# Kernel tuning notes

Hardware: AMD Instinct MI355X
Metric: run time of the kernel (lower is better)

## Reference

```python
import jax, jax.numpy as jnp
import numpy as np

N_NODES = 100000
N_EDGES = 1600000
D = 32  # atom and bond feature dim


def _mlp(x, W1, b1, W2, b2, W3, b3):
    # fff: Linear(in,128) -> ReLU -> Linear(128,64) -> ReLU -> Linear(64,32)
    h = jax.nn.relu(x @ W1 + b1)
    h = jax.nn.relu(h @ W2 + b2)
    return h @ W3 + b3


def _init_mlp(key, in_dim):
    ks = jax.random.split(key, 3)
    def lin(k, fan_in, fan_out):
        bound = 1.0 / np.sqrt(fan_in)
        kw, kb = jax.random.split(k)
        W = jax.random.uniform(kw, (fan_in, fan_out), jnp.float32, -bound, bound)
        b = jax.random.uniform(kb, (fan_out,), jnp.float32, -bound, bound)
        return W, b
    W1, b1 = lin(ks[0], in_dim, 128)
    W2, b2 = lin(ks[1], 128, 64)
    W3, b3 = lin(ks[2], 64, 32)
    return W1, b1, W2, b2, W3, b3


def setup_inputs() -> dict:
    key = jax.random.key(0)
    k_bonds, k_a1, k_a2, k_atoms, k_e, k_v = jax.random.split(key, 6)
    inp = {
        "bonds": jax.random.normal(k_bonds, (N_EDGES, D), jnp.float32),
        "bond_atom_1": jax.random.randint(k_a1, (N_EDGES,), 0, N_NODES, jnp.int64),
        "bond_atom_2": jax.random.randint(k_a2, (N_EDGES,), 0, N_NODES, jnp.int64),
        "atoms": jax.random.normal(k_atoms, (N_NODES, D), jnp.float32),
    }
    We1, be1, We2, be2, We3, be3 = _init_mlp(k_e, 96)
    Wv1, bv1, Wv2, bv2, Wv3, bv3 = _init_mlp(k_v, 64)
    inp.update(We1=We1, be1=be1, We2=We2, be2=be2, We3=We3, be3=be3,
               Wv1=Wv1, bv1=bv1, Wv2=Wv2, bv2=bv2, Wv3=Wv3, bv3=bv3)
    return inp


def reference(bonds, bond_atom_1, bond_atom_2, atoms,
              We1, be1, We2, be2, We3, be3,
              Wv1, bv1, Wv2, bv2, Wv3, bv3):
    # Edge update: gather endpoint atom features, concat with bond feats, MLP
    atom1 = atoms[bond_atom_1]                    # [E, D]
    atom2 = atoms[bond_atom_2]                    # [E, D]
    e_in = jnp.concatenate([atom1, atom2, bonds], axis=1)  # [E, 3D]
    new_bonds = _mlp(e_in, We1, be1, We2, be2, We3, be3)    # [E, 32]

    # Node update: scatter-mean new bond features onto target atoms
    # (PyG default flow aggregates messages at edge_index[1] == bond_atom_2)
    n = atoms.shape[0]
    seg_sum = jax.ops.segment_sum(new_bonds, bond_atom_2, num_segments=n)
    counts = jax.ops.segment_sum(jnp.ones((new_bonds.shape[0],), new_bonds.dtype),
                                 bond_atom_2, num_segments=n)
    mean_bonds = seg_sum / jnp.maximum(counts, 1.0)[:, None]  # [N, 32]

    v_in = jnp.concatenate([mean_bonds, atoms], axis=1)        # [N, 64]
    new_atoms = _mlp(v_in, Wv1, bv1, Wv2, bv2, Wv3, bv3)       # [N, 32]
    return (new_atoms, new_bonds)
```

## Files before the change

kernel.cpp:

```cpp
#include <hip/hip_runtime.h>
#include <hip/hip_bf16.h>

#define NN 100000
#define NE 1600000
#define NB_SCAN 391
#define ETILES 12500
#define EGRID 768
#define NGRID 1024

typedef __attribute__((ext_vector_type(8))) short bfrag8;
typedef __attribute__((ext_vector_type(4))) float f32x4;
typedef __attribute__((ext_vector_type(8))) unsigned short us8;
typedef __attribute__((ext_vector_type(4))) unsigned int u32x4;

__device__ __forceinline__ unsigned short f2bf(float f) {
  unsigned int u = __float_as_uint(f);
  u += 0x7fffu + ((u >> 16) & 1u);
  return (unsigned short)(u >> 16);
}

__device__ __forceinline__ unsigned int pk2(float a, float b) {
  unsigned int r;
  asm("v_cvt_pk_bf16_f32 %0, %1, %2" : "=v"(r) : "v"(a), "v"(b));
  return r;
}

__device__ __forceinline__ uint2 pk4(float v0, float v1, float v2, float v3) {
  return make_uint2(pk2(v0, v1), pk2(v2, v3));
}

__device__ __forceinline__ bfrag8 pack8(float4 a, float4 b) {
  union { u32x4 u; bfrag8 f; } c;
  c.u[0] = pk2(a.x, a.y); c.u[1] = pk2(a.z, a.w);
  c.u[2] = pk2(b.x, b.y); c.u[3] = pk2(b.z, b.w);
  return c.f;
}

__device__ __forceinline__ bfrag8 as_frag(us8 v) {
  union { us8 u; bfrag8 f; } c;
  c.u = v;
  return c.f;
}

__device__ __forceinline__ bfrag8 as_frag_u(u32x4 v) {
  union { u32x4 u; bfrag8 f; } c;
  c.u = v;
  return c.f;
}

__device__ __forceinline__ unsigned int sh(unsigned int v, int src) {
  return (unsigned int)__shfl((int)v, src, 64);
}

__device__ __forceinline__ float bl(unsigned int u) { return __uint_as_float(u << 16); }
__device__ __forceinline__ float bh(unsigned int u) { return __uint_as_float(u & 0xffff0000u); }

__device__ __forceinline__ f32x4 mfma16(bfrag8 a, bfrag8 b, f32x4 c) {
  return __builtin_amdgcn_mfma_f32_16x16x32_bf16(a, b, c, 0, 0, 0);
}

__device__ __forceinline__ void gload_lds16(const void* g, void* l) {
  __builtin_amdgcn_global_load_lds(
      (const __attribute__((address_space(1))) unsigned int*)g,
      (__attribute__((address_space(3))) unsigned int*)l, 16, 0, 0);
}

__global__ void prep(const float* __restrict__ atoms, unsigned short* __restrict__ atoms_bf,
                     const int* __restrict__ a2, int* __restrict__ cnt,
                     const float* __restrict__ We1, const float* __restrict__ We2,
                     const float* __restrict__ We3, const float* __restrict__ Wv1,
                     const float* __restrict__ Wv2, const float* __restrict__ Wv3,
                     unsigned short* __restrict__ wp) {
  const int b = blockIdx.x, tid = threadIdx.x;
  if (b < 3125) {
    const int i = b * 256 + tid;
    float4 v = *(const float4*)(atoms + (size_t)i * 4);
    *(uint2*)(atoms_bf + (size_t)i * 4) = pk4(v.x, v.y, v.z, v.w);
  } else if (b < 3125 + 6250) {
    const int e = (b - 3125) * 256 + tid;
    if (e < NE) atomicAdd(&cnt[a2[e]], 1);
  } else {
    const int i = (b - 9375) * 256 + tid;
    const float* src; int base, N;
    if (i < 12288)      { src = We1; base = 0;     N = 128; }
    else if (i < 20480) { src = We2; base = 12288; N = 64;  }
    else if (i < 22528) { src = We3; base = 20480; N = 32;  }
    else if (i < 30720) { src = Wv1; base = 22528; N = 128; }
    else if (i < 38912) { src = Wv2; base = 30720; N = 64;  }
    else                { src = Wv3; base = 38912; N = 32;  }
    const int il = i - base;
    const int j = il & 7, gc = il >> 3;
    const int c = gc % N, g = gc / N;
    wp[i] = f2bf(src[(g * 8 + j) * N + c]);
  }
}

__global__ void scan_blocks(const int* __restrict__ cnt, int* __restrict__ off,
                            int* __restrict__ bsum) {
  __shared__ int s[256];
  const int t = threadIdx.x;
  const int idx = blockIdx.x * 256 + t;
  int v = (idx < NN) ? cnt[idx] : 0;
  s[t] = v;
  __syncthreads();
  for (int d = 1; d < 256; d <<= 1) {
    int x = (t >= d) ? s[t - d] : 0;
    __syncthreads();
    s[t] += x;
    __syncthreads();
  }
  if (idx < NN) off[idx] = s[t] - v;
  if (t == 255) bsum[blockIdx.x] = s[255];
}

__global__ void scan_finalize(int* __restrict__ off, const int* __restrict__ bsum,
                              int* __restrict__ cursor) {
  __shared__ int red[256];
  const int b = blockIdx.x, t = threadIdx.x;
  int s = 0;
  for (int k = t; k < b; k += 256) s += bsum[k];
  red[t] = s;
  __syncthreads();
  for (int d = 128; d > 0; d >>= 1) {
    if (t < d) red[t] += red[t + d];
    __syncthreads();
  }
  const int base = red[0];
  const int idx = b * 256 + t;
  if (idx < NN) {
    int o = off[idx] + base;
    off[idx] = o;
    cursor[idx] = o;
  }
  if (idx == 0) off[NN] = NE;
}

__global__ void fill_k(const int* __restrict__ a2, int* __restrict__ cursor,
                       int* __restrict__ buf, int mode) {
  int e = blockIdx.x * 256 + threadIdx.x;
  if (e < NE) {
    int p = atomicAdd(&cursor[a2[e]], 1);
    if (mode) buf[e] = p;
    else buf[p] = e;
  }
}

template <int FAST>
__global__ __launch_bounds__(256, 3) void edge_kernel(
    const float* __restrict__ bonds, const int* __restrict__ a1p, const int* __restrict__ a2p,
    const unsigned short* __restrict__ atoms_bf,
    const float* __restrict__ be1, const float* __restrict__ be2, const float* __restrict__ be3,
    const unsigned short* __restrict__ wpack,
    float* __restrict__ new_bonds,
    const int* __restrict__ pos, unsigned short* __restrict__ nb_bf) {
  __shared__ unsigned short sW[22528];
  __shared__ float sB1[128], sB2[64], sB3[32];

  const int tid = threadIdx.x;
  const int lane = tid & 63, wv = tid >> 6;
  const int cl = lane & 15, q = lane >> 4;
  const int esub = wv * 32 + cl;
  const int srcA = cl + ((q & 1) << 5);
  const int srcB = srcA + 16;
  const bool hi = (lane & 32) != 0;

  {
    const char* src = (const char*)wpack;
    char* dst = (char*)sW;
#pragma unroll
    for (int i = 0; i < 11; ++i) {
      const int c = i * 4 + wv;
      gload_lds16(src + c * 1024 + lane * 16, dst + c * 1024);
    }
  }
  if (tid < 128) sB1[tid] = be1[tid];
  else if (tid < 192) sB2[tid - 128] = be2[tid - 128];
  else if (tid < 224) sB3[tid - 192] = be3[tid - 192];

  int tile = blockIdx.x;
  us8 ra1[2], ra2[2];
  float4 rb[2][2];
  int ia1n[2], ia2n[2];

#pragma unroll
  for (int t = 0; t < 2; ++t) {
    const int e = tile * 128 + esub + t * 16;
    const int ia1 = a1p[e], ia2 = a2p[e];
    ra1[t] = *(const us8*)(atoms_bf + (size_t)ia1 * 32 + q * 8);
    ra2[t] = *(const us8*)(atoms_bf + (size_t)ia2 * 32 + q * 8);
    const float* bp = bonds + (size_t)e * 32 + q * 8;
    rb[t][0] = *(const float4*)(bp);
    rb[t][1] = *(const float4*)(bp + 4);
  }
  {
    int tn = tile + EGRID; if (tn >= ETILES) tn = tile;
#pragma unroll
    for (int t = 0; t < 2; ++t) {
      const int e = tn * 128 + esub + t * 16;
      ia1n[t] = a1p[e]; ia2n[t] = a2p[e];
    }
  }
  __syncthreads();

  for (; tile < ETILES; tile += EGRID) {
    bfrag8 xb0[2], xb1[2], xb2[2];
#pragma unroll
    for (int t = 0; t < 2; ++t) {
      xb0[t] = as_frag(ra1[t]);
      xb1[t] = as_frag(ra2[t]);
      xb2[t] = pack8(rb[t][0], rb[t][1]);
    }
    const int tn = (tile + EGRID < ETILES) ? tile + EGRID : tile;
#pragma unroll
    for (int t = 0; t < 2; ++t) {
      ra1[t] = *(const us8*)(atoms_bf + (size_t)ia1n[t] * 32 + q * 8);
      ra2[t] = *(const us8*)(atoms_bf + (size_t)ia2n[t] * 32 + q * 8);
      const int e = tn * 128 + esub + t * 16;
      const float* bp = bonds + (size_t)e * 32 + q * 8;
      rb[t][0] = *(const float4*)(bp);
      rb[t][1] = *(const float4*)(bp + 4);
    }
    {
      int tnn = tile + 2 * EGRID; if (tnn >= ETILES) tnn = tn;
#pragma unroll
      for (int t = 0; t < 2; ++t) {
        const int e = tnn * 128 + esub + t * 16;
        ia1n[t] = a1p[e]; ia2n[t] = a2p[e];
      }
    }

    unsigned int hp[2][8][2];
#pragma unroll
    for (int rt = 0; rt < 8; ++rt) {
      const unsigned short* wa = &sW[(q * 128 + rt * 16 + cl) * 8];
      bfrag8 w0 = *(const bfrag8*)(wa);
      bfrag8 w1 = *(const bfrag8*)(wa + 4096);
      bfrag8 w2 = *(const bfrag8*)(wa + 8192);
      const int c0 = rt * 16 + q * 4;
#pragma unroll
      for (int t = 0; t < 2; ++t) {
        f32x4 acc = {0.f, 0.f, 0.f, 0.f};
        acc = mfma16(w0, xb0[t], acc);
        acc = mfma16(w1, xb1[t], acc);
        acc = mfma16(w2, xb2[t], acc);
        hp[t][rt][0] = pk2(fmaxf(acc[0] + sB1[c0 + 0], 0.f),
                           fmaxf(acc[1] + sB1[c0 + 1], 0.f));
        hp[t][rt][1] = pk2(fmaxf(acc[2] + sB1[c0 + 2], 0.f),
                           fmaxf(acc[3] + sB1[c0 + 3], 0.f));
      }
    }

    f32x4 acc2[2][4];
#pragma unroll
    for (int t = 0; t < 2; ++t)
#pragma unroll
      for (int rt = 0; rt < 4; ++rt) acc2[t][rt] = (f32x4){0.f, 0.f, 0.f, 0.f};
#pragma unroll
    for (int ks = 0; ks < 4; ++ks) {
      bfrag8 hb[2];
#pragma unroll
      for (int t = 0; t < 2; ++t) {
        u32x4 bw;
        unsigned int x, y;
        x = sh(hp[t][2 * ks][0], srcA); y = sh(hp[t][2 * ks + 1][0], srcA); bw[0] = hi ? y : x;
        x = sh(hp[t][2 * ks][1], srcA); y = sh(hp[t][2 * ks + 1][1], srcA); bw[1] = hi ? y : x;
        x = sh(hp[t][2 * ks][0], srcB); y = sh(hp[t][2 * ks + 1][0], srcB); bw[2] = hi ? y : x;
        x = sh(hp[t][2 * ks][1], srcB); y = sh(hp[t][2 * ks + 1][1], srcB); bw[3] = hi ? y : x;
        hb[t] = as_frag_u(bw);
      }
#pragma unroll
      for (int rt = 0; rt < 4; ++rt) {
        bfrag8 w = *(const bfrag8*)&sW[12288 + ks * 2048 + (q * 64 + rt * 16 + cl) * 8];
#pragma unroll
        for (int t = 0; t < 2; ++t) acc2[t][rt] = mfma16(w, hb[t], acc2[t][rt]);
      }
    }
    unsigned int hp2[2][4][2];
#pragma unroll
    for (int rt = 0; rt < 4; ++rt) {
      const int c0 = rt * 16 + q * 4;
#pragma unroll
      for (int t = 0; t < 2; ++t) {
        hp2[t][rt][0] = pk2(fmaxf(acc2[t][rt][0] + sB2[c0 + 0], 0.f),
                            fmaxf(acc2[t][rt][1] + sB2[c0 + 1], 0.f));
        hp2[t][rt][1] = pk2(fmaxf(acc2[t][rt][2] + sB2[c0 + 2], 0.f),
                            fmaxf(acc2[t][rt][3] + sB2[c0 + 3], 0.f));
      }
    }

    f32x4 acc3[2][2];
#pragma unroll
    for (int t = 0; t < 2; ++t)
#pragma unroll
      for (int rt = 0; rt < 2; ++rt) acc3[t][rt] = (f32x4){0.f, 0.f, 0.f, 0.f};
#pragma unroll
    for (int ks = 0; ks < 2; ++ks) {
      bfrag8 gb[2];
#pragma unroll
      for (int t = 0; t < 2; ++t) {
        u32x4 bw;
        unsigned int x, y;
        x = sh(hp2[t][2 * ks][0], srcA); y = sh(hp2[t][2 * ks + 1][0], srcA); bw[0] = hi ? y : x;
        x = sh(hp2[t][2 * ks][1], srcA); y = sh(hp2[t][2 * ks + 1][1], srcA); bw[1] = hi ? y : x;
        x = sh(hp2[t][2 * ks][0], srcB); y = sh(hp2[t][2 * ks + 1][0], srcB); bw[2] = hi ? y : x;
        x = sh(hp2[t][2 * ks][1], srcB); y = sh(hp2[t][2 * ks + 1][1], srcB); bw[3] = hi ? y : x;
        gb[t] = as_frag_u(bw);
      }
#pragma unroll
      for (int rt = 0; rt < 2; ++rt) {
        bfrag8 w = *(const bfrag8*)&sW[20480 + ks * 1024 + (q * 32 + rt * 16 + cl) * 8];
#pragma unroll
        for (int t = 0; t < 2; ++t) acc3[t][rt] = mfma16(w, gb[t], acc3[t][rt]);
      }
    }

    unsigned int hp3[2][2][2];
#pragma unroll
    for (int rt = 0; rt < 2; ++rt) {
      const int c0 = rt * 16 + q * 4;
#pragma unroll
      for (int t = 0; t < 2; ++t) {
        float4 o;
        o.x = acc3[t][rt][0] + sB3[c0 + 0];
        o.y = acc3[t][rt][1] + sB3[c0 + 1];
        o.z = acc3[t][rt][2] + sB3[c0 + 2];
        o.w = acc3[t][rt][3] + sB3[c0 + 3];
        const int e = tile * 128 + esub + t * 16;
        *(float4*)(new_bonds + (size_t)e * 32 + c0) = o;
        if (FAST) {
          hp3[t][rt][0] = pk2(o.x, o.y);
          hp3[t][rt][1] = pk2(o.z, o.w);
        }
      }
    }
    if (FAST) {
#pragma unroll
      for (int t = 0; t < 2; ++t) {
        const int slot = pos[tile * 128 + wv * 32 + t * 16 + cl];
        u32x4 W;
        unsigned int x, y;
        x = sh(hp3[t][0][0], srcA); y = sh(hp3[t][1][0], srcA); W[0] = hi ? y : x;
        x = sh(hp3[t][0][1], srcA); y = sh(hp3[t][1][1], srcA); W[1] = hi ? y : x;
        x = sh(hp3[t][0][0], srcB); y = sh(hp3[t][1][0], srcB); W[2] = hi ? y : x;
        x = sh(hp3[t][0][1], srcB); y = sh(hp3[t][1][1], srcB); W[3] = hi ? y : x;
        *(u32x4*)(nb_bf + (size_t)slot * 32 + q * 8) = W;
      }
    }
  }
}

__global__ __launch_bounds__(256, 8) void gather_seq(
    const int* __restrict__ off, const unsigned short* __restrict__ nb_bf,
    unsigned short* __restrict__ mean_bf) {
  const int gt = blockIdx.x * 256 + threadIdx.x;
  const int n = gt >> 3, sl = gt & 7;
  const int o0 = off[n], o1 = off[n + 1];
  const int deg = o1 - o0;
  float s0 = 0.f, s1 = 0.f, s2 = 0.f, s3 = 0.f;
  const unsigned short* p = nb_bf + (size_t)o0 * 32 + sl * 4;
  int i = 0;
  for (; i + 1 < deg; i += 2) {
    uint2 a = *(const uint2*)(p);
    uint2 b = *(const uint2*)(p + 32);
    p += 64;
    s0 += bl(a.x) + bl(b.x); s1 += bh(a.x) + bh(b.x);
    s2 += bl(a.y) + bl(b.y); s3 += bh(a.y) + bh(b.y);
  }
  if (i < deg) {
    uint2 a = *(const uint2*)(p);
    s0 += bl(a.x); s1 += bh(a.x); s2 += bl(a.y); s3 += bh(a.y);
  }
  const float inv = 1.0f / fmaxf((float)deg, 1.0f);
  *(uint2*)(mean_bf + (size_t)n * 32 + sl * 4) =
      make_uint2(pk2(s0 * inv, s1 * inv), pk2(s2 * inv, s3 * inv));
}

__global__ __launch_bounds__(256, 8) void gather_rand(
    const int* __restrict__ off, const int* __restrict__ csr,
    const float* __restrict__ new_bonds, float* __restrict__ mean_f32) {
  const int tid = blockIdx.x * 256 + threadIdx.x;
  const int n = tid >> 3, sl = tid & 7;
  const int o0 = off[n], o1 = off[n + 1];
  float4 s0 = {0.f, 0.f, 0.f, 0.f}, s1 = {0.f, 0.f, 0.f, 0.f};
  int i = o0;
  for (; i + 1 < o1; i += 2) {
    const int ea = csr[i], eb = csr[i + 1];
    float4 a = *(const float4*)(new_bonds + (size_t)ea * 32 + sl * 4);
    float4 b = *(const float4*)(new_bonds + (size_t)eb * 32 + sl * 4);
    s0.x += a.x; s0.y += a.y; s0.z += a.z; s0.w += a.w;
    s1.x += b.x; s1.y += b.y; s1.z += b.z; s1.w += b.w;
  }
  if (i < o1) {
    const int ea = csr[i];
    float4 a = *(const float4*)(new_bonds + (size_t)ea * 32 + sl * 4);
    s0.x += a.x; s0.y += a.y; s0.z += a.z; s0.w += a.w;
  }
  const float inv = 1.0f / fmaxf((float)(o1 - o0), 1.0f);
  float4 m;
  m.x = (s0.x + s1.x) * inv;
  m.y = (s0.y + s1.y) * inv;
  m.z = (s0.z + s1.z) * inv;
  m.w = (s0.w + s1.w) * inv;
  *(float4*)(mean_f32 + (size_t)n * 32 + sl * 4) = m;
}

template <int MODE>
__global__ __launch_bounds__(256, 4) void node_mlp(
    const unsigned short* __restrict__ atoms_bf,
    const float* __restrict__ bv1, const float* __restrict__ bv2, const float* __restrict__ bv3,
    const unsigned short* __restrict__ wpack,
    const void* __restrict__ mean_src, float* __restrict__ new_atoms) {
  __shared__ unsigned short sW[18432];
  __shared__ float sB1[128], sB2[64], sB3[32];
  __shared__ unsigned short sV[64 * 72];
  __shared__ unsigned short sH1[64 * 136];

  const int tid = threadIdx.x;
  const int lane = tid & 63, wv = tid >> 6;
  const int cl = lane & 15, q = lane >> 4;
  const int nl = tid >> 2, l4 = tid & 3;

  {
    const uint4* src = (const uint4*)wpack;
    uint4* dst = (uint4*)sW;
#pragma unroll
    for (int i = 0; i < 9; ++i) dst[tid + i * 256] = src[tid + i * 256];
  }
  if (tid < 128) sB1[tid] = bv1[tid];
  if (tid < 64) sB2[tid] = bv2[tid];
  if (tid < 32) sB3[tid] = bv3[tid];

  for (int n0 = blockIdx.x * 64; n0 < NN; n0 += NGRID * 64) {
    __syncthreads();

    {
      const int n = n0 + nl;
      if (n < NN) {
        if (l4 < 2) {
          if (MODE == 1) {
            const unsigned short* mp = (const unsigned short*)mean_src + (size_t)n * 32 + l4 * 16;
            *(us8*)&sV[nl * 72 + l4 * 16] = *(const us8*)(mp);
            *(us8*)&sV[nl * 72 + l4 * 16 + 8] = *(const us8*)(mp + 8);
          } else {
            const float* sp = (const float*)mean_src + (size_t)n * 32 + l4 * 16;
            float4 a = *(const float4*)(sp);
            float4 b = *(const float4*)(sp + 4);
            float4 c = *(const float4*)(sp + 8);
            float4 d = *(const float4*)(sp + 12);
            uint4 o0, o1;
            o0.x = pk2(a.x, a.y); o0.y = pk2(a.z, a.w);
            o0.z = pk2(b.x, b.y); o0.w = pk2(b.z, b.w);
            o1.x = pk2(c.x, c.y); o1.y = pk2(c.z, c.w);
            o1.z = pk2(d.x, d.y); o1.w = pk2(d.z, d.w);
            *(uint4*)&sV[nl * 72 + l4 * 16] = o0;
            *(uint4*)&sV[nl * 72 + l4 * 16 + 8] = o1;
          }
        } else {
          const unsigned short* ap = atoms_bf + (size_t)n * 32 + (l4 - 2) * 16;
          *(us8*)&sV[nl * 72 + 32 + (l4 - 2) * 16] = *(const us8*)(ap);
          *(us8*)&sV[nl * 72 + 32 + (l4 - 2) * 16 + 8] = *(const us8*)(ap + 8);
        }
      } else {
        us8 z = {0, 0, 0, 0, 0, 0, 0, 0};
        *(us8*)&sV[nl * 72 + l4 * 16] = z;
        *(us8*)&sV[nl * 72 + l4 * 16 + 8] = z;
      }
    }
    __syncthreads();

    const int nt = wv * 16;
    const int ng = n0 + nt + cl;

    bfrag8 vb0 = *(const bfrag8*)&sV[(nt + cl) * 72 + q * 8];
    bfrag8 vb1 = *(const bfrag8*)&sV[(nt + cl) * 72 + 32 + q * 8];
#pragma unroll
    for (int rt = 0; rt < 8; ++rt) {
      f32x4 acc = {0.f, 0.f, 0.f, 0.f};
      acc = mfma16(*(const bfrag8*)&sW[(q * 128 + rt * 16 + cl) * 8], vb0, acc);
      acc = mfma16(*(const bfrag8*)&sW[4096 + (q * 128 + rt * 16 + cl) * 8], vb1, acc);
      const int c0 = rt * 16 + q * 4;
      uint2 hv = pk4(fmaxf(acc[0] + sB1[c0 + 0], 0.f),
                     fmaxf(acc[1] + sB1[c0 + 1], 0.f),
                     fmaxf(acc[2] + sB1[c0 + 2], 0.f),
                     fmaxf(acc[3] + sB1[c0 + 3], 0.f));
      *(uint2*)&sH1[(nt + cl) * 136 + c0] = hv;
    }
    __syncthreads();

    bfrag8 hb[4];
    {
      const unsigned short* hr = &sH1[(nt + cl) * 136 + q * 8];
#pragma unroll
      for (int ks = 0; ks < 4; ++ks) hb[ks] = *(const bfrag8*)(hr + ks * 32);
    }
    __syncthreads();
#pragma unroll
    for (int rt = 0; rt < 4; ++rt) {
      f32x4 acc = {0.f, 0.f, 0.f, 0.f};
#pragma unroll
      for (int ks = 0; ks < 4; ++ks)
        acc = mfma16(*(const bfrag8*)&sW[8192 + ks * 2048 + (q * 64 + rt * 16 + cl) * 8], hb[ks], acc);
      const int c0 = rt * 16 + q * 4;
      uint2 hv = pk4(fmaxf(acc[0] + sB2[c0 + 0], 0.f),
                     fmaxf(acc[1] + sB2[c0 + 1], 0.f),
                     fmaxf(acc[2] + sB2[c0 + 2], 0.f),
                     fmaxf(acc[3] + sB2[c0 + 3], 0.f));
      *(uint2*)&sV[(nt + cl) * 72 + c0] = hv;
    }
    __syncthreads();

    bfrag8 gb0 = *(const bfrag8*)&sV[(nt + cl) * 72 + q * 8];
    bfrag8 gb1 = *(const bfrag8*)&sV[(nt + cl) * 72 + 32 + q * 8];
    if (ng < NN) {
      float* outp = new_atoms + (size_t)ng * 32;
#pragma unroll
      for (int rt = 0; rt < 2; ++rt) {
        f32x4 acc = {0.f, 0.f, 0.f, 0.f};
        acc = mfma16(*(const bfrag8*)&sW[16384 + (q * 32 + rt * 16 + cl) * 8], gb0, acc);
        acc = mfma16(*(const bfrag8*)&sW[16384 + 1024 + (q * 32 + rt * 16 + cl) * 8], gb1, acc);
        const int c0 = rt * 16 + q * 4;
        float4 o;
        o.x = acc[0] + sB3[c0 + 0];
        o.y = acc[1] + sB3[c0 + 1];
        o.z = acc[2] + sB3[c0 + 2];
        o.w = acc[3] + sB3[c0 + 3];
        *(float4*)(outp + c0) = o;
      }
    }
  }
}

extern "C" void kernel_launch(void* const* d_in, const int* in_sizes, int n_in,
                              void* d_out, int out_size, void* d_ws, size_t ws_size,
                              hipStream_t stream) {
  const float* bonds = (const float*)d_in[0];
  const int* a1 = (const int*)d_in[1];
  const int* a2 = (const int*)d_in[2];
  const float* atoms = (const float*)d_in[3];
  const float* We1 = (const float*)d_in[4];
  const float* be1 = (const float*)d_in[5];
  const float* We2 = (const float*)d_in[6];
  const float* be2 = (const float*)d_in[7];
  const float* We3 = (const float*)d_in[8];
  const float* be3 = (const float*)d_in[9];
  const float* Wv1 = (const float*)d_in[10];
  const float* bv1 = (const float*)d_in[11];
  const float* Wv2 = (const float*)d_in[12];
  const float* bv2 = (const float*)d_in[13];
  const float* Wv3 = (const float*)d_in[14];
  const float* bv3 = (const float*)d_in[15];

  float* out = (float*)d_out;
  float* new_atoms = out;
  float* new_bonds = out + (size_t)NN * 32;

  char* ws = (char*)d_ws;
  int* cnt    = (int*)(ws + 0);
  int* off    = (int*)(ws + 400000);
  int* bsum   = (int*)(ws + 800016);
  unsigned short* wp = (unsigned short*)(ws + 802064);
  int* poscsr = (int*)(ws + 883984);
  unsigned short* atoms_bf = (unsigned short*)(ws + 7283984);
  unsigned short* mean_bf  = (unsigned short*)(ws + 13683984);
  unsigned short* nb_bf    = (unsigned short*)(ws + 20083984);

  const int fast = (ws_size >= (size_t)122483984) ? 1 : 0;

  hipMemsetAsync(cnt, 0, (size_t)NN * 4, stream);

  prep<<<9535, 256, 0, stream>>>(atoms, atoms_bf, a2, cnt,
                                 We1, We2, We3, Wv1, Wv2, Wv3, wp);

  scan_blocks<<<NB_SCAN, 256, 0, stream>>>(cnt, off, bsum);
  scan_finalize<<<NB_SCAN, 256, 0, stream>>>(off, bsum, cnt);
  fill_k<<<(NE + 255) / 256, 256, 0, stream>>>(a2, cnt, poscsr, fast);

  if (fast) {
    edge_kernel<1><<<EGRID, 256, 0, stream>>>(bonds, a1, a2, atoms_bf, be1, be2, be3, wp,
                                              new_bonds, poscsr, nb_bf);
    gather_seq<<<NN * 8 / 256, 256, 0, stream>>>(off, nb_bf, mean_bf);
    node_mlp<1><<<NGRID, 256, 0, stream>>>(atoms_bf, bv1, bv2, bv3, wp + 22528,
                                           mean_bf, new_atoms);
  } else {
    edge_kernel<0><<<EGRID, 256, 0, stream>>>(bonds, a1, a2, atoms_bf, be1, be2, be3, wp,
                                              new_bonds, nullptr, nullptr);
    gather_rand<<<NN * 8 / 256, 256, 0, stream>>>(off, poscsr, new_bonds, new_atoms);
    node_mlp<0><<<NGRID, 256, 0, stream>>>(atoms_bf, bv1, bv2, bv3, wp + 22528,
                                           new_atoms, new_atoms);
  }
}
```

Measured before the change: 442.5 us.

## Stage bf16 edge outputs through LDS and keep layer-3 weights in registers

Layer-3 weight fragments now load once into registers instead of being re-read from LDS every tile, which frees LDS. The bf16 scatter of new bond features is staged in a padded LDS buffer, and 128 threads each write a full 64-byte row to its sorted slot, replacing the per-lane cross-lane shuffle path. The slot index for the next tile is prefetched. This adds two block barriers per tile and extra register pressure under launch_bounds(256,3).

```diff
diff --git a/kernel.cpp b/kernel.cpp
--- a/kernel.cpp
+++ b/kernel.cpp
@@ -153,8 +153,9 @@
     const unsigned short* __restrict__ wpack,
     float* __restrict__ new_bonds,
     const int* __restrict__ pos, unsigned short* __restrict__ nb_bf) {
-  __shared__ unsigned short sW[22528];
+  __shared__ unsigned short sW[20480];
   __shared__ float sB1[128], sB2[64], sB3[32];
+  __shared__ unsigned short sOut[128 * 40];
 
   const int tid = threadIdx.x;
   const int lane = tid & 63, wv = tid >> 6;
@@ -168,11 +169,17 @@
     const char* src = (const char*)wpack;
     char* dst = (char*)sW;
 #pragma unroll
-    for (int i = 0; i < 11; ++i) {
+    for (int i = 0; i < 10; ++i) {
       const int c = i * 4 + wv;
       gload_lds16(src + c * 1024 + lane * 16, dst + c * 1024);
     }
   }
+  bfrag8 w3[2][2];
+#pragma unroll
+  for (int ks = 0; ks < 2; ++ks)
+#pragma unroll
+    for (int rt = 0; rt < 2; ++rt)
+      w3[ks][rt] = *(const bfrag8*)(wpack + 20480 + ks * 1024 + (q * 32 + rt * 16 + cl) * 8);
   if (tid < 128) sB1[tid] = be1[tid];
   else if (tid < 192) sB2[tid - 128] = be2[tid - 128];
   else if (tid < 224) sB3[tid - 192] = be3[tid - 192];
@@ -181,6 +188,7 @@
   us8 ra1[2], ra2[2];
   float4 rb[2][2];
   int ia1n[2], ia2n[2];
+  int slotc = 0;
 
 #pragma unroll
   for (int t = 0; t < 2; ++t) {
@@ -192,6 +200,7 @@
     rb[t][0] = *(const float4*)(bp);
     rb[t][1] = *(const float4*)(bp + 4);
   }
+  if (FAST && tid < 128) slotc = pos[tile * 128 + tid];
   {
     int tn = tile + EGRID; if (tn >= ETILES) tn = tile;
 #pragma unroll
@@ -220,6 +229,8 @@
       rb[t][0] = *(const float4*)(bp);
       rb[t][1] = *(const float4*)(bp + 4);
     }
+    int slotn = 0;
+    if (FAST && tid < 128) slotn = pos[tn * 128 + tid];
     {
       int tnn = tile + 2 * EGRID; if (tnn >= ETILES) tnn = tn;
 #pragma unroll
@@ -307,14 +318,11 @@
         gb[t] = as_frag_u(bw);
       }
 #pragma unroll
-      for (int rt = 0; rt < 2; ++rt) {
-        bfrag8 w = *(const bfrag8*)&sW[20480 + ks * 1024 + (q * 32 + rt * 16 + cl) * 8];
-#pragma unroll
-        for (int t = 0; t < 2; ++t) acc3[t][rt] = mfma16(w, gb[t], acc3[t][rt]);
-      }
-    }
-
-    unsigned int hp3[2][2][2];
+      for (int rt = 0; rt < 2; ++rt)
+#pragma unroll
+        for (int t = 0; t < 2; ++t) acc3[t][rt] = mfma16(w3[ks][rt], gb[t], acc3[t][rt]);
+    }
+
 #pragma unroll
     for (int rt = 0; rt < 2; ++rt) {
       const int c0 = rt * 16 + q * 4;
@@ -328,23 +336,21 @@
         const int e = tile * 128 + esub + t * 16;
         *(float4*)(new_bonds + (size_t)e * 32 + c0) = o;
         if (FAST) {
-          hp3[t][rt][0] = pk2(o.x, o.y);
-          hp3[t][rt][1] = pk2(o.z, o.w);
+          *(uint2*)&sOut[(esub + t * 16) * 40 + c0] =
+              make_uint2(pk2(o.x, o.y), pk2(o.z, o.w));
         }
       }
     }
     if (FAST) {
-#pragma unroll
-      for (int t = 0; t < 2; ++t) {
-        const int slot = pos[tile * 128 + wv * 32 + t * 16 + cl];
-        u32x4 W;
-        unsigned int x, y;
-        x = sh(hp3[t][0][0], srcA); y = sh(hp3[t][1][0], srcA); W[0] = hi ? y : x;
-        x = sh(hp3[t][0][1], srcA); y = sh(hp3[t][1][1], srcA); W[1] = hi ? y : x;
-        x = sh(hp3[t][0][0], srcB); y = sh(hp3[t][1][0], srcB); W[2] = hi ? y : x;
-        x = sh(hp3[t][0][1], srcB); y = sh(hp3[t][1][1], srcB); W[3] = hi ? y : x;
-        *(u32x4*)(nb_bf + (size_t)slot * 32 + q * 8) = W;
-      }
+      __syncthreads();
+      if (tid < 128) {
+        const u32x4* src = (const u32x4*)&sOut[tid * 40];
+        u32x4* dst = (u32x4*)(nb_bf + (size_t)slotc * 32);
+#pragma unroll
+        for (int k = 0; k < 4; ++k) dst[k] = src[k];
+      }
+      slotc = slotn;
+      __syncthreads();
     }
   }
 }
```

Result: faster. 392.8 us (-11.2%).
